# Optimization experiments

Hardware: AMD Instinct MI355X
Metric: run time of the kernel (lower is better)

The kernel has to match this reference:

```python
import jax, jax.numpy as jnp
import numpy as np

B, S, E, H, D = 64, 512, 512, 8, 64  # batch, n_steps, embedding_size, head_count, QKV_dim

def setup_inputs() -> dict:
    key = jax.random.key(0)
    ks = jax.random.split(key, 7)
    x = jax.random.normal(ks[0], (B, S, E), dtype=jnp.float32)
    mask = jax.random.randint(ks[1], (B, S), 0, 2).astype(jnp.float32)  # 1 = masked out
    WQ = jax.random.normal(ks[2], (H, E, D), dtype=jnp.float32) * 0.1
    WK = jax.random.normal(ks[3], (H, E, D), dtype=jnp.float32) * 0.1
    WV = jax.random.normal(ks[4], (H, E, D), dtype=jnp.float32) * 0.1
    BE = jax.random.normal(ks[5], (S, E), dtype=jnp.float32) * 0.1
    WO = jax.random.normal(ks[6], (H * D, E), dtype=jnp.float32) * 0.1
    return {"x": x, "mask": mask, "WQ": WQ, "WK": WK, "WV": WV, "BE": BE, "WO": WO}

def reference(x, mask, WQ, WK, WV, BE, WO):
    # add learned positional bias
    h = x + BE  # [B,S,E]
    # per-head projections, vectorized over heads
    Q = jnp.einsum('bse,hed->bhsd', h, WQ)
    K = jnp.einsum('bse,hed->bhsd', h, WK)
    V = jnp.einsum('bse,hed->bhsd', h, WV)
    # NOTE: original scales by sqrt(embedding_size), not sqrt(QKV_dim)
    scores = jnp.einsum('bhsd,bhtd->bhst', Q, K) / np.sqrt(E).astype(np.float32)
    # additive mask trick: mask tiled over query dim, key positions masked where mask==1
    scores = scores - mask[:, None, None, :] * 1e10
    alpha = jax.nn.softmax(scores, axis=-1)  # [B,H,S,S]
    attn = jnp.einsum('bhst,bhtd->bhsd', alpha, V)  # [B,H,S,D]
    # concat heads along feature dim -> [B,S,H*D], then output projection
    attn = jnp.transpose(attn, (0, 2, 1, 3)).reshape(x.shape[0], x.shape[1], -1)
    return attn @ WO  # [B,S,E]
```

## Files before the change

kernel.cpp:

```cpp
#include <hip/hip_runtime.h>
#include <hip/hip_bf16.h>


#define Bn 64
#define Sn 512
#define En 512
#define Hn 8
#define Dn 64

typedef __attribute__((ext_vector_type(8))) short s8v;
typedef __attribute__((ext_vector_type(4))) float f4v;

__device__ __forceinline__ unsigned short f2bf(float f) {
    union { float f; unsigned int u; } v; v.f = f;
    unsigned int u = v.u;
    u += 0x7fffu + ((u >> 16) & 1u);
    return (unsigned short)(u >> 16);
}

__device__ __forceinline__ void async16(const unsigned short* g, unsigned short* l) {
    __builtin_amdgcn_global_load_lds((const __attribute__((address_space(1))) void*)g,
                                     (__attribute__((address_space(3))) void*)l, 16, 0, 0);
}
__device__ __forceinline__ void async4(const float* g, float* l) {
    __builtin_amdgcn_global_load_lds((const __attribute__((address_space(1))) void*)g,
                                     (__attribute__((address_space(3))) void*)l, 4, 0, 0);
}

__global__ __launch_bounds__(256) void prep_all(const float* __restrict__ x,
                                                const float* __restrict__ BE,
                                                const float* __restrict__ WQ,
                                                const float* __restrict__ WK,
                                                const float* __restrict__ WV,
                                                const float* __restrict__ WO,
                                                unsigned short* __restrict__ hbf,
                                                unsigned short* __restrict__ Wqkvt,
                                                unsigned short* __restrict__ WOt) {
    int bid = blockIdx.x;
    if (bid < 16384) {
        int i = (bid * 256 + threadIdx.x) * 4;
        int se = i % (Sn * En);
        float4 a = *(const float4*)(x + i);
        float4 b = *(const float4*)(BE + se);
        ushort4 o;
        o.x = f2bf(a.x + b.x); o.y = f2bf(a.y + b.y);
        o.z = f2bf(a.z + b.z); o.w = f2bf(a.w + b.w);
        *(ushort4*)(hbf + i) = o;
    } else {
        int idx = (bid - 16384) * 256 + threadIdx.x;
        const int NW = 3 * Hn * Dn * En;
        if (idx < NW) {
            int e = idx & 511;
            int d = (idx >> 9) & 63;
            int h = (idx >> 15) & 7;
            int m = idx >> 18;
            const float* W = (m == 0) ? WQ : (m == 1) ? WK : WV;
            Wqkvt[idx] = f2bf(W[(h * En + e) * Dn + d]);
        } else {
            int j = idx - NW;
            int n = j & 511;
            int e = j >> 9;
            WOt[j] = f2bf(WO[n * En + e]);
        }
    }
}

__device__ __forceinline__ void mfma8(const s8v& a0k0, const s8v& a0k1,
                                      const s8v& a1k0, const s8v& a1k1,
                                      f4v* acc0, f4v* acc1,
                                      const s8v (&bq)[4][2], bool sw) {
    if (sw) {
#pragma unroll
        for (int n = 0; n < 4; n++) {
            acc0[n] = __builtin_amdgcn_mfma_f32_16x16x32_bf16(bq[n][0], a0k0, acc0[n], 0, 0, 0);
            acc0[n] = __builtin_amdgcn_mfma_f32_16x16x32_bf16(bq[n][1], a0k1, acc0[n], 0, 0, 0);
            acc1[n] = __builtin_amdgcn_mfma_f32_16x16x32_bf16(bq[n][0], a1k0, acc1[n], 0, 0, 0);
            acc1[n] = __builtin_amdgcn_mfma_f32_16x16x32_bf16(bq[n][1], a1k1, acc1[n], 0, 0, 0);
        }
    } else {
#pragma unroll
        for (int n = 0; n < 4; n++) {
            acc0[n] = __builtin_amdgcn_mfma_f32_16x16x32_bf16(a0k0, bq[n][0], acc0[n], 0, 0, 0);
            acc0[n] = __builtin_amdgcn_mfma_f32_16x16x32_bf16(a0k1, bq[n][1], acc0[n], 0, 0, 0);
            acc1[n] = __builtin_amdgcn_mfma_f32_16x16x32_bf16(a1k0, bq[n][0], acc1[n], 0, 0, 0);
            acc1[n] = __builtin_amdgcn_mfma_f32_16x16x32_bf16(a1k1, bq[n][1], acc1[n], 0, 0, 0);
        }
    }
}

__global__ __launch_bounds__(512, 2) void qkv_gemm(const unsigned short* __restrict__ hbf,
                                                   const unsigned short* __restrict__ Wqkvt,
                                                   unsigned short* __restrict__ Qo,
                                                   unsigned short* __restrict__ Ko,
                                                   unsigned short* __restrict__ Vt) {
    __shared__ __align__(16) unsigned short As[2][16384];
    __shared__ __align__(16) unsigned short Bs[2][16384];

    int lin = blockIdx.y * 6 + blockIdx.x;
    int swz = (lin & 7) * 96 + (lin >> 3);
    int mb = swz / 6, nbv = swz - mb * 6;

    int tid = threadIdx.x;
    int w = tid >> 6, lane = tid & 63, quad = lane >> 4, l16 = lane & 15, l7 = l16 & 7;
    int wr = w >> 2, wcn = w & 3;

    const unsigned short* Ag = hbf + (size_t)mb * 256 * 512;
    const unsigned short* Bg = Wqkvt + (size_t)nbv * 256 * 512;

    int colbase = nbv * 256 + wcn * 64;
    bool swapQK = colbase < 1024;

    int ha = (lane >> 3) & 1;
    int ca = w * 4 + (lane >> 4);
    int aG0 = (ca + 128 * ha) * 512 + ((lane & 7) ^ (ca & 7)) * 8;
    int rb0 = w * 8 + (lane >> 3);
    int bG0 = rb0 * 512 + ((lane & 7) ^ (rb0 & 7)) * 8;

    int arow = 2 * l16 + wr;
    int aseg0 = (quad ^ l7) * 8;
    int aseg1 = ((4 + quad) ^ l7) * 8;

    f4v acc[8][4];
#pragma unroll
    for (int i = 0; i < 8; i++)
#pragma unroll
        for (int n = 0; n < 4; n++) acc[i][n] = (f4v){0.f, 0.f, 0.f, 0.f};
    s8v bq[4][2];

#define STA8(o_, p_, kt_) async16(Ag + aG0 + (p_) * 16384 + (kt_) * 64, &As[o_][(p_) * 4096 + w * 512])
#define STB8(o_, q_, kt_) async16(Bg + bG0 + (q_) * 32768 + (kt_) * 64, &Bs[o_][(q_) * 4096 + w * 512])

#define PHASE8(P, STAGES, GATE)                                                   \
    do {                                                                          \
        if ((P) == 0) {                                                           \
            _Pragma("unroll")                                                     \
            for (int n = 0; n < 4; n++) {                                         \
                int br = (wcn * 64 + n * 16 + l16) * 64;                          \
                bq[n][0] = *(const s8v*)&Bs_s[br + aseg0];                        \
                bq[n][1] = *(const s8v*)&Bs_s[br + aseg1];                        \
            }                                                                     \
        }                                                                         \
        s8v a0k0 = *(const s8v*)&As_s[(((P) * 2 + 0) * 32 + arow) * 64 + aseg0];  \
        s8v a0k1 = *(const s8v*)&As_s[(((P) * 2 + 0) * 32 + arow) * 64 + aseg1];  \
        s8v a1k0 = *(const s8v*)&As_s[(((P) * 2 + 1) * 32 + arow) * 64 + aseg0];  \
        s8v a1k1 = *(const s8v*)&As_s[(((P) * 2 + 1) * 32 + arow) * 64 + aseg1];  \
        STAGES;                                                                   \
        __builtin_amdgcn_s_barrier();                                             \
        asm volatile("s_waitcnt lgkmcnt(0)" ::: "memory");                        \
        __builtin_amdgcn_s_setprio(1);                                            \
        mfma8(a0k0, a0k1, a1k0, a1k1, &acc[(P) * 2][0], &acc[(P) * 2 + 1][0], bq, swapQK); \
        __builtin_amdgcn_s_setprio(0);                                            \
        GATE;                                                                     \
        __builtin_amdgcn_s_barrier();                                             \
    } while (0)

    STB8(0, 0, 0); STB8(0, 1, 0); STB8(0, 2, 0); STB8(0, 3, 0);
    STA8(0, 0, 0); STA8(0, 1, 0); STA8(0, 2, 0); STA8(0, 3, 0);
    asm volatile("s_waitcnt vmcnt(0)" ::: "memory");
    __builtin_amdgcn_s_barrier();

    for (int k = 0; k < 7; k++) {
        int s = k & 1, o = s ^ 1, kt = k + 1;
        const unsigned short* As_s = &As[s][0];
        const unsigned short* Bs_s = &Bs[s][0];
        PHASE8(0, { STB8(o, 0, kt); STB8(o, 1, kt); STA8(o, 0, kt); },
               asm volatile("s_waitcnt vmcnt(6)" ::: "memory"));
        PHASE8(1, { STB8(o, 2, kt); STA8(o, 1, kt); },
               asm volatile("s_waitcnt vmcnt(6)" ::: "memory"));
        PHASE8(2, { STB8(o, 3, kt); STA8(o, 2, kt); },
               asm volatile("s_waitcnt vmcnt(7)" ::: "memory"));
        PHASE8(3, { STA8(o, 3, kt); },
               asm volatile("s_waitcnt vmcnt(2)" ::: "memory"));
    }
    {
        const unsigned short* As_s = &As[1][0];
        const unsigned short* Bs_s = &Bs[1][0];
        PHASE8(0, {}, asm volatile("s_waitcnt vmcnt(3)" ::: "memory"));
        PHASE8(1, {}, asm volatile("s_waitcnt vmcnt(1)" ::: "memory"));
        PHASE8(2, {}, asm volatile("s_waitcnt vmcnt(0)" ::: "memory"));
        PHASE8(3, {}, (void)0);
    }
#undef PHASE8
#undef STA8
#undef STB8

    int mat = colbase >> 9;
    int h = (colbase >> 6) & 7;
    int b_idx = mb >> 1;
    const float qscale = 0.06375873f;

    if (swapQK) {
        unsigned short* op = (mat == 0) ? Qo : Ko;
        float sc = (mat == 0) ? qscale : 1.0f;
#pragma unroll
        for (int mi = 0; mi < 8; mi++)
#pragma unroll
            for (int n = 0; n < 4; n++) {
                int s_ = (mb & 1) * 256 + wr * 128 + mi * 16 + l16;
                int d0 = n * 16 + quad * 4;
                ushort4 pk;
                pk.x = f2bf(acc[mi][n][0] * sc);
                pk.y = f2bf(acc[mi][n][1] * sc);
                pk.z = f2bf(acc[mi][n][2] * sc);
                pk.w = f2bf(acc[mi][n][3] * sc);
                *(ushort4*)&op[(size_t)((b_idx * Hn + h) * Sn + s_) * Dn + d0] = pk;
            }
    } else {
#pragma unroll
        for (int mi = 0; mi < 8; mi++)
#pragma unroll
            for (int n = 0; n < 4; n++) {
                int d = n * 16 + l16;
                int srow = (mb & 1) * 256 + wr * 128 + mi * 16 + quad * 4;
                ushort4 pk;
                pk.x = f2bf(acc[mi][n][0]); pk.y = f2bf(acc[mi][n][1]);
                pk.z = f2bf(acc[mi][n][2]); pk.w = f2bf(acc[mi][n][3]);
                *(ushort4*)&Vt[(size_t)((b_idx * Hn + h) * Dn + d) * Sn + srow] = pk;
            }
    }
}

__global__ __launch_bounds__(256) void attn_kernel(const unsigned short* __restrict__ Q,
                                                   const unsigned short* __restrict__ K,
                                                   const unsigned short* __restrict__ Vt,
                                                   const float* __restrict__ mask,
                                                   unsigned short* __restrict__ attn) {
    int qhalf = blockIdx.x, bh = blockIdx.y;
    int h = bh & 7, b = bh >> 3;
    __shared__ __align__(16) unsigned short Kc[64 * 64];
    __shared__ __align__(16) unsigned short Vc[64 * 64];
    __shared__ __align__(16) unsigned short Ps[4][4 * 16 * 64];
    __shared__ float maskv[64];
    int tid = threadIdx.x;
    int w = tid >> 6, lane = tid & 63, quad = lane >> 4, l16 = lane & 15;
    int l7 = l16 & 7;

    const unsigned short* Qg = Q + (size_t)(bh * Sn + qhalf * 256) * Dn;
    const unsigned short* Kg = K + (size_t)(bh * Sn) * Dn;
    const unsigned short* Vg = Vt + (size_t)(bh * Dn) * Sn;

    s8v aq[4][2];
#pragma unroll
    for (int i = 0; i < 4; i++)
#pragma unroll
        for (int ks = 0; ks < 2; ks++)
            aq[i][ks] = *(const s8v*)&Qg[((w * 4 + i) * 16 + l16) * 64 + ks * 32 + quad * 8];

    f4v acc[4][4];
    float psum[4] = {0.f, 0.f, 0.f, 0.f};
#pragma unroll
    for (int i = 0; i < 4; i++)
#pragma unroll
        for (int n = 0; n < 4; n++) acc[i][n] = (f4v){0.f, 0.f, 0.f, 0.f};

    int srow0 = w * 16 + (lane >> 3);
    int srow1 = srow0 + 8;
    int gseg0 = ((lane & 7) ^ (srow0 & 7)) * 8;
    int gseg1 = ((lane & 7) ^ (srow1 & 7)) * 8;
    unsigned short* kdst0 = &Kc[(w * 16) * 64];
    unsigned short* kdst1 = &Kc[(w * 16 + 8) * 64];
    unsigned short* vdst0 = &Vc[(w * 16) * 64];
    unsigned short* vdst1 = &Vc[(w * 16 + 8) * 64];

    unsigned short* Pw = Ps[w];
    int wbase = l16 * 64 + (quad & 1) * 4;
    const float cM = -1.4426950409e10f;

    for (int kc = 0; kc < 8; kc++) {
        __syncthreads();
        async16(Kg + (kc * 64 + srow0) * 64 + gseg0, kdst0);
        async16(Kg + (kc * 64 + srow1) * 64 + gseg1, kdst1);
        async16(Vg + srow0 * 512 + kc * 64 + gseg0, vdst0);
        async16(Vg + srow1 * 512 + kc * 64 + gseg1, vdst1);
        if (w == 0) async4(mask + b * Sn + kc * 64 + lane, maskv);
        __syncthreads();

#pragma unroll
        for (int n = 0; n < 4; n++) {
            s8v bk0 = *(const s8v*)&Kc[(n * 16 + l16) * 64 + (quad ^ l7) * 8];
            s8v bk1 = *(const s8v*)&Kc[(n * 16 + l16) * 64 + ((4 + quad) ^ l7) * 8];
            float4 mv = *(const float4*)&maskv[n * 16 + quad * 4];
            float m0 = mv.x * cM, m1 = mv.y * cM, m2 = mv.z * cM, m3 = mv.w * cM;
            int wseg = ((n * 2 + (quad >> 1)) ^ l7) * 8;
            f4v sacc[4];
#pragma unroll
            for (int i = 0; i < 4; i++) {
                sacc[i] = __builtin_amdgcn_mfma_f32_16x16x32_bf16(
                              bk0, aq[i][0], (f4v){0.f, 0.f, 0.f, 0.f}, 0, 0, 0);
                sacc[i] = __builtin_amdgcn_mfma_f32_16x16x32_bf16(
                              bk1, aq[i][1], sacc[i], 0, 0, 0);
            }
#pragma unroll
            for (int i = 0; i < 4; i++) {
                unsigned int u0 = __float_as_uint(__builtin_amdgcn_exp2f(sacc[i][0] + m0));
                unsigned int u1 = __float_as_uint(__builtin_amdgcn_exp2f(sacc[i][1] + m1));
                unsigned int u2 = __float_as_uint(__builtin_amdgcn_exp2f(sacc[i][2] + m2));
                unsigned int u3 = __float_as_uint(__builtin_amdgcn_exp2f(sacc[i][3] + m3));
                psum[i] += __uint_as_float(u0 & 0xffff0000u) + __uint_as_float(u1 & 0xffff0000u)
                         + __uint_as_float(u2 & 0xffff0000u) + __uint_as_float(u3 & 0xffff0000u);
                uint2 pk;
                pk.x = (u0 >> 16) | (u1 & 0xffff0000u);
                pk.y = (u2 >> 16) | (u3 & 0xffff0000u);
                *(uint2*)&Pw[(i << 10) + wbase + wseg] = pk;
            }
        }

#pragma unroll
        for (int ks = 0; ks < 2; ks++) {
            int sw = ((ks * 4 + quad) ^ l7) * 8;
            s8v ap[4];
#pragma unroll
            for (int i = 0; i < 4; i++)
                ap[i] = *(const s8v*)&Pw[(i << 10) + l16 * 64 + sw];
#pragma unroll
            for (int n = 0; n < 4; n++) {
                s8v bv = *(const s8v*)&Vc[(n * 16 + l16) * 64 + sw];
#pragma unroll
                for (int i = 0; i < 4; i++)
                    acc[i][n] = __builtin_amdgcn_mfma_f32_16x16x32_bf16(ap[i], bv, acc[i][n], 0, 0, 0);
            }
        }
    }

#pragma unroll
    for (int i = 0; i < 4; i++) {
        float s = psum[i];
        s += __shfl_xor(s, 16, 64);
        s += __shfl_xor(s, 32, 64);
        float inv[4];
#pragma unroll
        for (int r = 0; r < 4; r++)
            inv[r] = 1.0f / __shfl(s, quad * 4 + r, 64);
#pragma unroll
        for (int n = 0; n < 4; n++)
#pragma unroll
            for (int r = 0; r < 4; r++) {
                int query = qhalf * 256 + (w * 4 + i) * 16 + quad * 4 + r;
                int col = h * 64 + n * 16 + l16;
                attn[(size_t)(b * Sn + query) * (Hn * Dn) + col] = f2bf(acc[i][n][r] * inv[r]);
            }
    }
}

__global__ __launch_bounds__(512, 2) void outproj(const unsigned short* __restrict__ attn,
                                                  const unsigned short* __restrict__ WOt,
                                                  float* __restrict__ out) {
    __shared__ __align__(16) unsigned short As[2][16384];
    __shared__ __align__(16) unsigned short Bs[2][16384];

    int lin = blockIdx.y * 2 + blockIdx.x;
    int swz = (lin & 7) * 32 + (lin >> 3);
    int mb = swz >> 1, nbv = swz & 1;

    int tid = threadIdx.x;
    int w = tid >> 6, lane = tid & 63, quad = lane >> 4, l16 = lane & 15, l7 = l16 & 7;
    int wr = w >> 2, wcn = w & 3;

    const unsigned short* Ag = attn + (size_t)mb * 256 * 512;
    const unsigned short* Bg = WOt + (size_t)nbv * 256 * 512;

    int ha = (lane >> 3) & 1;
    int ca = w * 4 + (lane >> 4);
    int aG0 = (ca + 128 * ha) * 512 + ((lane & 7) ^ (ca & 7)) * 8;
    int rb0 = w * 8 + (lane >> 3);
    int bG0 = rb0 * 512 + ((lane & 7) ^ (rb0 & 7)) * 8;

    int arow = 2 * l16 + wr;
    int aseg0 = (quad ^ l7) * 8;
    int aseg1 = ((4 + quad) ^ l7) * 8;

    f4v acc[8][4];
#pragma unroll
    for (int i = 0; i < 8; i++)
#pragma unroll
        for (int n = 0; n < 4; n++) acc[i][n] = (f4v){0.f, 0.f, 0.f, 0.f};
    s8v bq[4][2];

#define STA8(o_, p_, kt_) async16(Ag + aG0 + (p_) * 16384 + (kt_) * 64, &As[o_][(p_) * 4096 + w * 512])
#define STB8(o_, q_, kt_) async16(Bg + bG0 + (q_) * 32768 + (kt_) * 64, &Bs[o_][(q_) * 4096 + w * 512])

#define PHASE8(P, STAGES, GATE)                                                   \
    do {                                                                          \
        if ((P) == 0) {                                                           \
            _Pragma("unroll")                                                     \
            for (int n = 0; n < 4; n++) {                                         \
                int br = (wcn * 64 + n * 16 + l16) * 64;                          \
                bq[n][0] = *(const s8v*)&Bs_s[br + aseg0];                        \
                bq[n][1] = *(const s8v*)&Bs_s[br + aseg1];                        \
            }                                                                     \
        }                                                                         \
        s8v a0k0 = *(const s8v*)&As_s[(((P) * 2 + 0) * 32 + arow) * 64 + aseg0];  \
        s8v a0k1 = *(const s8v*)&As_s[(((P) * 2 + 0) * 32 + arow) * 64 + aseg1];  \
        s8v a1k0 = *(const s8v*)&As_s[(((P) * 2 + 1) * 32 + arow) * 64 + aseg0];  \
        s8v a1k1 = *(const s8v*)&As_s[(((P) * 2 + 1) * 32 + arow) * 64 + aseg1];  \
        STAGES;                                                                   \
        __builtin_amdgcn_s_barrier();                                             \
        asm volatile("s_waitcnt lgkmcnt(0)" ::: "memory");                        \
        __builtin_amdgcn_s_setprio(1);                                            \
        mfma8(a0k0, a0k1, a1k0, a1k1, &acc[(P) * 2][0], &acc[(P) * 2 + 1][0], bq, true); \
        __builtin_amdgcn_s_setprio(0);                                            \
        GATE;                                                                     \
        __builtin_amdgcn_s_barrier();                                             \
    } while (0)

    STB8(0, 0, 0); STB8(0, 1, 0); STB8(0, 2, 0); STB8(0, 3, 0);
    STA8(0, 0, 0); STA8(0, 1, 0); STA8(0, 2, 0); STA8(0, 3, 0);
    asm volatile("s_waitcnt vmcnt(0)" ::: "memory");
    __builtin_amdgcn_s_barrier();

    for (int k = 0; k < 7; k++) {
        int s = k & 1, o = s ^ 1, kt = k + 1;
        const unsigned short* As_s = &As[s][0];
        const unsigned short* Bs_s = &Bs[s][0];
        PHASE8(0, { STB8(o, 0, kt); STB8(o, 1, kt); STA8(o, 0, kt); },
               asm volatile("s_waitcnt vmcnt(6)" ::: "memory"));
        PHASE8(1, { STB8(o, 2, kt); STA8(o, 1, kt); },
               asm volatile("s_waitcnt vmcnt(6)" ::: "memory"));
        PHASE8(2, { STB8(o, 3, kt); STA8(o, 2, kt); },
               asm volatile("s_waitcnt vmcnt(7)" ::: "memory"));
        PHASE8(3, { STA8(o, 3, kt); },
               asm volatile("s_waitcnt vmcnt(2)" ::: "memory"));
    }
    {
        const unsigned short* As_s = &As[1][0];
        const unsigned short* Bs_s = &Bs[1][0];
        PHASE8(0, {}, asm volatile("s_waitcnt vmcnt(3)" ::: "memory"));
        PHASE8(1, {}, asm volatile("s_waitcnt vmcnt(1)" ::: "memory"));
        PHASE8(2, {}, asm volatile("s_waitcnt vmcnt(0)" ::: "memory"));
        PHASE8(3, {}, (void)0);
    }
#undef PHASE8
#undef STA8
#undef STB8

#pragma unroll
    for (int mi = 0; mi < 8; mi++)
#pragma unroll
        for (int n = 0; n < 4; n++) {
            int row = mb * 256 + wr * 128 + mi * 16 + l16;
            int col = nbv * 256 + wcn * 64 + n * 16 + quad * 4;
            float4 o;
            o.x = acc[mi][n][0]; o.y = acc[mi][n][1];
            o.z = acc[mi][n][2]; o.w = acc[mi][n][3];
            *(float4*)&out[(size_t)row * 512 + col] = o;
        }
}

extern "C" void kernel_launch(void* const* d_in, const int* in_sizes, int n_in,
                              void* d_out, int out_size, void* d_ws, size_t ws_size,
                              hipStream_t stream) {
    const float* x    = (const float*)d_in[0];
    const float* mask = (const float*)d_in[1];
    const float* WQ   = (const float*)d_in[2];
    const float* WK   = (const float*)d_in[3];
    const float* WV   = (const float*)d_in[4];
    const float* BE   = (const float*)d_in[5];
    const float* WO   = (const float*)d_in[6];
    float* out = (float*)d_out;

    char* ws = (char*)d_ws;
    unsigned short* hbf   = (unsigned short*)(ws);
    unsigned short* Wqkvt = (unsigned short*)(ws + 33554432);
    unsigned short* WOt   = (unsigned short*)(ws + 35127296);
    unsigned short* Qp    = (unsigned short*)(ws + 35651584);
    unsigned short* Kp    = (unsigned short*)(ws + 69206016);
    unsigned short* Vtp   = (unsigned short*)(ws + 102760448);
    unsigned short* attnp = (unsigned short*)(ws + 136314880);

    prep_all<<<20480, 256, 0, stream>>>(x, BE, WQ, WK, WV, WO, hbf, Wqkvt, WOt);
    qkv_gemm<<<dim3(6, 128), 512, 0, stream>>>(hbf, Wqkvt, Qp, Kp, Vtp);
    attn_kernel<<<dim3(2, 512), 256, 0, stream>>>(Qp, Kp, Vtp, mask, attnp);
    outproj<<<dim3(2, 128), 512, 0, stream>>>(attnp, WOt, out);
}
```

Before: 287.1 us.

## Process full query sequence per attention block with 8 waves sharing K/V tiles

The attention kernel now launches one 512-thread block per (batch, head) instead of two 256-thread blocks, so all 512 queries share each K/V tile load and halving global K/V traffic. Each wave loads one async segment per tile instead of two. The per-wave P staging buffer is halved by processing the four query subtiles in two passes of two, which interleaves the QK/exp and PV phases. The cost is fewer blocks (512) and heavier register and LDS occupancy pressure under launch_bounds(512,4).

```diff
diff --git a/kernel.cpp b/kernel.cpp
--- a/kernel.cpp
+++ b/kernel.cpp
@@ -220,22 +220,22 @@
     }
 }
 
-__global__ __launch_bounds__(256) void attn_kernel(const unsigned short* __restrict__ Q,
-                                                   const unsigned short* __restrict__ K,
-                                                   const unsigned short* __restrict__ Vt,
-                                                   const float* __restrict__ mask,
-                                                   unsigned short* __restrict__ attn) {
-    int qhalf = blockIdx.x, bh = blockIdx.y;
+__global__ __launch_bounds__(512, 4) void attn_kernel(const unsigned short* __restrict__ Q,
+                                                      const unsigned short* __restrict__ K,
+                                                      const unsigned short* __restrict__ Vt,
+                                                      const float* __restrict__ mask,
+                                                      unsigned short* __restrict__ attn) {
+    int bh = blockIdx.x;
     int h = bh & 7, b = bh >> 3;
     __shared__ __align__(16) unsigned short Kc[64 * 64];
     __shared__ __align__(16) unsigned short Vc[64 * 64];
-    __shared__ __align__(16) unsigned short Ps[4][4 * 16 * 64];
+    __shared__ __align__(16) unsigned short Ps[8][2 * 16 * 64];
     __shared__ float maskv[64];
     int tid = threadIdx.x;
     int w = tid >> 6, lane = tid & 63, quad = lane >> 4, l16 = lane & 15;
     int l7 = l16 & 7;
 
-    const unsigned short* Qg = Q + (size_t)(bh * Sn + qhalf * 256) * Dn;
+    const unsigned short* Qg = Q + (size_t)(bh * Sn) * Dn;
     const unsigned short* Kg = K + (size_t)(bh * Sn) * Dn;
     const unsigned short* Vg = Vt + (size_t)(bh * Dn) * Sn;
 
@@ -253,14 +253,10 @@
 #pragma unroll
         for (int n = 0; n < 4; n++) acc[i][n] = (f4v){0.f, 0.f, 0.f, 0.f};
 
-    int srow0 = w * 16 + (lane >> 3);
-    int srow1 = srow0 + 8;
-    int gseg0 = ((lane & 7) ^ (srow0 & 7)) * 8;
-    int gseg1 = ((lane & 7) ^ (srow1 & 7)) * 8;
-    unsigned short* kdst0 = &Kc[(w * 16) * 64];
-    unsigned short* kdst1 = &Kc[(w * 16 + 8) * 64];
-    unsigned short* vdst0 = &Vc[(w * 16) * 64];
-    unsigned short* vdst1 = &Vc[(w * 16 + 8) * 64];
+    int srow = w * 8 + (lane >> 3);
+    int gseg = ((lane & 7) ^ (srow & 7)) * 8;
+    unsigned short* kdst = &Kc[(w * 8) * 64];
+    unsigned short* vdst = &Vc[(w * 8) * 64];
 
     unsigned short* Pw = Ps[w];
     int wbase = l16 * 64 + (quad & 1) * 4;
@@ -268,56 +264,57 @@
 
     for (int kc = 0; kc < 8; kc++) {
         __syncthreads();
-        async16(Kg + (kc * 64 + srow0) * 64 + gseg0, kdst0);
-        async16(Kg + (kc * 64 + srow1) * 64 + gseg1, kdst1);
-        async16(Vg + srow0 * 512 + kc * 64 + gseg0, vdst0);
-        async16(Vg + srow1 * 512 + kc * 64 + gseg1, vdst1);
+        async16(Kg + (kc * 64 + srow) * 64 + gseg, kdst);
+        async16(Vg + srow * 512 + kc * 64 + gseg, vdst);
         if (w == 0) async4(mask + b * Sn + kc * 64 + lane, maskv);
         __syncthreads();
 
 #pragma unroll
-        for (int n = 0; n < 4; n++) {
-            s8v bk0 = *(const s8v*)&Kc[(n * 16 + l16) * 64 + (quad ^ l7) * 8];
-            s8v bk1 = *(const s8v*)&Kc[(n * 16 + l16) * 64 + ((4 + quad) ^ l7) * 8];
-            float4 mv = *(const float4*)&maskv[n * 16 + quad * 4];
-            float m0 = mv.x * cM, m1 = mv.y * cM, m2 = mv.z * cM, m3 = mv.w * cM;
-            int wseg = ((n * 2 + (quad >> 1)) ^ l7) * 8;
-            f4v sacc[4];
-#pragma unroll
-            for (int i = 0; i < 4; i++) {
-                sacc[i] = __builtin_amdgcn_mfma_f32_16x16x32_bf16(
-                              bk0, aq[i][0], (f4v){0.f, 0.f, 0.f, 0.f}, 0, 0, 0);
-                sacc[i] = __builtin_amdgcn_mfma_f32_16x16x32_bf16(
-                              bk1, aq[i][1], sacc[i], 0, 0, 0);
+        for (int p = 0; p < 2; p++) {
+#pragma unroll
+            for (int n = 0; n < 4; n++) {
+                s8v bk0 = *(const s8v*)&Kc[(n * 16 + l16) * 64 + (quad ^ l7) * 8];
+                s8v bk1 = *(const s8v*)&Kc[(n * 16 + l16) * 64 + ((4 + quad) ^ l7) * 8];
+                float4 mv = *(const float4*)&maskv[n * 16 + quad * 4];
+                float m0 = mv.x * cM, m1 = mv.y * cM, m2 = mv.z * cM, m3 = mv.w * cM;
+                int wseg = ((n * 2 + (quad >> 1)) ^ l7) * 8;
+                f4v sacc[2];
+#pragma unroll
+                for (int j = 0; j < 2; j++) {
+                    int i = p * 2 + j;
+                    sacc[j] = __builtin_amdgcn_mfma_f32_16x16x32_bf16(
+                                  bk0, aq[i][0], (f4v){0.f, 0.f, 0.f, 0.f}, 0, 0, 0);
+                    sacc[j] = __builtin_amdgcn_mfma_f32_16x16x32_bf16(
+                                  bk1, aq[i][1], sacc[j], 0, 0, 0);
+                }
+#pragma unroll
+                for (int j = 0; j < 2; j++) {
+                    unsigned int u0 = __float_as_uint(__builtin_amdgcn_exp2f(sacc[j][0] + m0));
+                    unsigned int u1 = __float_as_uint(__builtin_amdgcn_exp2f(sacc[j][1] + m1));
+                    unsigned int u2 = __float_as_uint(__builtin_amdgcn_exp2f(sacc[j][2] + m2));
+                    unsigned int u3 = __float_as_uint(__builtin_amdgcn_exp2f(sacc[j][3] + m3));
+                    psum[p * 2 + j] += __uint_as_float(u0 & 0xffff0000u) + __uint_as_float(u1 & 0xffff0000u)
+                                     + __uint_as_float(u2 & 0xffff0000u) + __uint_as_float(u3 & 0xffff0000u);
+                    uint2 pk;
+                    pk.x = (u0 >> 16) | (u1 & 0xffff0000u);
+                    pk.y = (u2 >> 16) | (u3 & 0xffff0000u);
+                    *(uint2*)&Pw[(j << 10) + wbase + wseg] = pk;
+                }
             }
 #pragma unroll
-            for (int i = 0; i < 4; i++) {
-                unsigned int u0 = __float_as_uint(__builtin_amdgcn_exp2f(sacc[i][0] + m0));
-                unsigned int u1 = __float_as_uint(__builtin_amdgcn_exp2f(sacc[i][1] + m1));
-                unsigned int u2 = __float_as_uint(__builtin_amdgcn_exp2f(sacc[i][2] + m2));
-                unsigned int u3 = __float_as_uint(__builtin_amdgcn_exp2f(sacc[i][3] + m3));
-                psum[i] += __uint_as_float(u0 & 0xffff0000u) + __uint_as_float(u1 & 0xffff0000u)
-                         + __uint_as_float(u2 & 0xffff0000u) + __uint_as_float(u3 & 0xffff0000u);
-                uint2 pk;
-                pk.x = (u0 >> 16) | (u1 & 0xffff0000u);
-                pk.y = (u2 >> 16) | (u3 & 0xffff0000u);
-                *(uint2*)&Pw[(i << 10) + wbase + wseg] = pk;
-            }
-        }
-
-#pragma unroll
-        for (int ks = 0; ks < 2; ks++) {
-            int sw = ((ks * 4 + quad) ^ l7) * 8;
-            s8v ap[4];
-#pragma unroll
-            for (int i = 0; i < 4; i++)
-                ap[i] = *(const s8v*)&Pw[(i << 10) + l16 * 64 + sw];
-#pragma unroll
-            for (int n = 0; n < 4; n++) {
-                s8v bv = *(const s8v*)&Vc[(n * 16 + l16) * 64 + sw];
-#pragma unroll
-                for (int i = 0; i < 4; i++)
-                    acc[i][n] = __builtin_amdgcn_mfma_f32_16x16x32_bf16(ap[i], bv, acc[i][n], 0, 0, 0);
+            for (int ks = 0; ks < 2; ks++) {
+                int sw = ((ks * 4 + quad) ^ l7) * 8;
+                s8v ap[2];
+#pragma unroll
+                for (int j = 0; j < 2; j++)
+                    ap[j] = *(const s8v*)&Pw[(j << 10) + l16 * 64 + sw];
+#pragma unroll
+                for (int n = 0; n < 4; n++) {
+                    s8v bv = *(const s8v*)&Vc[(n * 16 + l16) * 64 + sw];
+#pragma unroll
+                    for (int j = 0; j < 2; j++)
+                        acc[p * 2 + j][n] = __builtin_amdgcn_mfma_f32_16x16x32_bf16(ap[j], bv, acc[p * 2 + j][n], 0, 0, 0);
+                }
             }
         }
     }
@@ -335,7 +332,7 @@
         for (int n = 0; n < 4; n++)
 #pragma unroll
             for (int r = 0; r < 4; r++) {
-                int query = qhalf * 256 + (w * 4 + i) * 16 + quad * 4 + r;
+                int query = (w * 4 + i) * 16 + quad * 4 + r;
                 int col = h * 64 + n * 16 + l16;
                 attn[(size_t)(b * Sn + query) * (Hn * Dn) + col] = f2bf(acc[i][n][r] * inv[r]);
             }
@@ -469,6 +466,6 @@
 
     prep_all<<<20480, 256, 0, stream>>>(x, BE, WQ, WK, WV, WO, hbf, Wqkvt, WOt);
     qkv_gemm<<<dim3(6, 128), 512, 0, stream>>>(hbf, Wqkvt, Qp, Kp, Vtp);
-    attn_kernel<<<dim3(2, 512), 256, 0, stream>>>(Qp, Kp, Vtp, mask, attnp);
+    attn_kernel<<<512, 512, 0, stream>>>(Qp, Kp, Vtp, mask, attnp);
     outproj<<<dim3(2, 128), 512, 0, stream>>>(attnp, WOt, out);
 }
```

Result: slower. 396.6 us (+38.1%).
